# Kernel optimization log

Measured on AMD Instinct MI355X. Metric: run time of the kernel, lower is better.

The kernel has to match this reference:

```python
import jax, jax.numpy as jnp
import numpy as np

NB, H, C, HID, EMB = 4, 12, 1024, 768, 512
E, M, L, SPAN = 22, 4, 16, 32
TD, INTER = 20, 256
NN = E + E * M + L
NREL, NLAYERS = 3, 4

def _build_adj():
    # static relational adjacency: r0 entity<->its mentions, r1 mention<->co-entity mention, r2 mention<->link
    A = np.zeros((NREL, NN, NN), np.float32)
    for e in range(E):
        for m in range(M):
            mi = E + e * M + m
            A[0, e, mi] = A[0, mi, e] = 1.0
            for m2 in range(M):
                if m2 != m:
                    A[1, mi, E + e * M + m2] = 1.0
            li = E + E * M + ((e * M + m) % L)
            A[2, mi, li] = A[2, li, mi] = 1.0
    A = A / (A.sum(-1, keepdims=True) + 1e-5)
    return jnp.asarray(A)

_ADJ = _build_adj()
_TYPES = np.concatenate([np.zeros(E, np.int32), np.ones(E * M, np.int32), np.full(L, 2, np.int32)])

def _forward(sequence_output, attention, W_trans, b_trans, type_embed,
             rgcn_Wrel0, rgcn_Wself0, rgcn_Wrel, rgcn_Wself,
             fs_w1, fs_b1, fs_g1, fs_be1, fs_w2, fs_b2, fs_g2, fs_be2,
             fc_w1, fc_b1, fc_g1, fc_be1, fc_w2, fc_b2, fc_g2, fc_be2,
             cr_w1, cr_b1, cr_w2, cr_b2, cr_w3, cr_b3,
             mention_idx, link_start):
    n = sequence_output.shape[0]
    b = jnp.arange(n)[:, None, None]
    seq = sequence_output @ W_trans + b_trans            # [n,C,EMB] extractor_trans
    attq = attention.transpose(0, 2, 1, 3)               # [n,C,H,C] query-major
    # --- make_graph: mention / entity nodes (gather + logsumexp pooling) ---
    m_rep = seq[b, mention_idx]                          # [n,E,M,EMB]
    m_att = attq[b, mention_idx]                         # [n,E,M,H,C]
    e_rep = jax.nn.logsumexp(m_rep, axis=2)              # [n,E,EMB]
    e_att = m_att.mean(axis=2)                           # [n,E,H,C]
    # --- link nodes: attention-weighted span pooling ---
    idx = link_start[:, :, None] + jnp.arange(SPAN)      # [n,L,SPAN]
    span = seq[b, idx]                                   # [n,L,SPAN,EMB]
    att_rows = attq[b, idx]                              # [n,L,SPAN,H,C]
    col_idx = jnp.broadcast_to(idx[:, :, None, None, :], (n, L, SPAN, H, SPAN))
    block = jnp.take_along_axis(att_rows, col_idx, axis=4).mean(axis=3)  # [n,L,SPAN,SPAN]
    link_rep = jnp.einsum('nlst,nltd->nld', block, span) / SPAN          # [n,L,EMB]
    # --- node matrix + type embedding ---
    nodes = jnp.concatenate([e_rep, m_rep.reshape(n, E * M, EMB), link_rep], axis=1)
    tfeat = jnp.broadcast_to(type_embed[_TYPES][None], (n, NN, TD))
    h = jnp.concatenate([nodes, tfeat], axis=-1)         # [n,NN,EMB+TD]
    # --- RGCN ---
    def rgcn_layer(hh, Wrel, Wself):
        msg = jnp.einsum('rij,njd,rdo->nio', _ADJ, hh, Wrel)
        return jax.nn.relu(msg + hh @ Wself)
    h = rgcn_layer(h, rgcn_Wrel0, rgcn_Wself0)
    for l in range(NLAYERS - 1):
        h = rgcn_layer(h, rgcn_Wrel[l], rgcn_Wself[l])
    # --- relation_map: structure + attention-weighted context ---
    entity_stru = h[:, :E]                               # [n,E,EMB]
    ea = e_att.mean(axis=2)                              # [n,E,C]
    ea = ea / (ea.sum(-1, keepdims=True) + 1e-5)
    e_ctx = jnp.einsum('nec,ncd->ned', ea, seq)          # [n,E,EMB]
    ec = entity_stru + e_ctx
    fmap = (ec[:, :, None, :] * ec[:, None, :, :]).transpose(0, 3, 1, 2)  # [n,EMB,E,E]
    # --- SE fusion (fusion_s / fusion_c, BN in eval form) ---
    conv1x1 = lambda x, w, bb: jnp.einsum('nchw,oc->nohw', x, w) + bb[None, :, None, None]
    bn = lambda x, g, be: x * g[None, :, None, None] + be[None, :, None, None]
    s = bn(conv1x1(jax.nn.relu(bn(conv1x1(fmap, fs_w1, fs_b1), fs_g1, fs_be1)), fs_w2, fs_b2), fs_g2, fs_be2)
    pooled = fmap.mean(axis=(2, 3), keepdims=True)
    cb = bn(conv1x1(jax.nn.relu(bn(conv1x1(pooled, fc_w1, fc_b1), fc_g1, fc_be1)), fc_w2, fc_b2), fc_g2, fc_be2)
    fused = fmap * jax.nn.sigmoid(s + cb)
    # --- conv_reason 5x5 blocks ---
    dn = ('NCHW', 'OIHW', 'NCHW')
    conv = lambda x, w, bb: jax.lax.conv_general_dilated(x, w, (1, 1), 'SAME', dimension_numbers=dn) + bb[None, :, None, None]
    r = jax.nn.relu(conv(fused, cr_w1, cr_b1))
    r = jax.nn.relu(conv(r, cr_w2, cr_b2))
    return jax.nn.relu(conv(r, cr_w3, cr_b3))            # [n,EMB,E,E]

def setup_inputs():
    key = jax.random.key(0)
    ks = jax.random.split(key, 24)
    p = lambda k, sh: jax.random.normal(k, sh, jnp.float32) * 0.02
    z = lambda sh: jnp.zeros(sh, jnp.float32)
    o = lambda sh: jnp.ones(sh, jnp.float32)
    return {
        'sequence_output': jax.random.normal(ks[0], (NB, C, HID), jnp.float32),
        'attention': jax.random.uniform(ks[1], (NB, H, C, C), jnp.float32),
        'W_trans': p(ks[2], (HID, EMB)), 'b_trans': z((EMB,)),
        'type_embed': p(ks[3], (3, TD)),
        'rgcn_Wrel0': p(ks[4], (NREL, EMB + TD, EMB)), 'rgcn_Wself0': p(ks[5], (EMB + TD, EMB)),
        'rgcn_Wrel': p(ks[6], (NLAYERS - 1, NREL, EMB, EMB)), 'rgcn_Wself': p(ks[7], (NLAYERS - 1, EMB, EMB)),
        'fs_w1': p(ks[8], (INTER, EMB)), 'fs_b1': z((INTER,)), 'fs_g1': o((INTER,)), 'fs_be1': z((INTER,)),
        'fs_w2': p(ks[9], (EMB, INTER)), 'fs_b2': z((EMB,)), 'fs_g2': o((EMB,)), 'fs_be2': z((EMB,)),
        'fc_w1': p(ks[10], (INTER, EMB)), 'fc_b1': z((INTER,)), 'fc_g1': o((INTER,)), 'fc_be1': z((INTER,)),
        'fc_w2': p(ks[11], (EMB, INTER)), 'fc_b2': z((EMB,)), 'fc_g2': o((EMB,)), 'fc_be2': z((EMB,)),
        'cr_w1': p(ks[12], (INTER, EMB, 5, 5)), 'cr_b1': z((INTER,)),
        'cr_w2': p(ks[13], (INTER, INTER, 5, 5)), 'cr_b2': z((INTER,)),
        'cr_w3': p(ks[14], (EMB, INTER, 5, 5)), 'cr_b3': z((EMB,)),
        'mention_idx': jax.random.randint(ks[15], (NB, E, M), 0, C),
        'link_start': jnp.sort(jax.random.randint(ks[16], (NB, L), 0, C - SPAN), axis=-1),
    }

def reference(sequence_output, attention, W_trans, b_trans, type_embed,
              rgcn_Wrel0, rgcn_Wself0, rgcn_Wrel, rgcn_Wself,
              fs_w1, fs_b1, fs_g1, fs_be1, fs_w2, fs_b2, fs_g2, fs_be2,
              fc_w1, fc_b1, fc_g1, fc_be1, fc_w2, fc_b2, fc_g2, fc_be2,
              cr_w1, cr_b1, cr_w2, cr_b2, cr_w3, cr_b3,
              mention_idx, link_start):
    return _forward(sequence_output, attention, W_trans, b_trans, type_embed,
                    rgcn_Wrel0, rgcn_Wself0, rgcn_Wrel, rgcn_Wself,
                    fs_w1, fs_b1, fs_g1, fs_be1, fs_w2, fs_b2, fs_g2, fs_be2,
                    fc_w1, fc_b1, fc_g1, fc_be1, fc_w2, fc_b2, fc_g2, fc_be2,
                    cr_w1, cr_b1, cr_w2, cr_b2, cr_w3, cr_b3,
                    mention_idx, link_start)
```

## Files before the change

### kernel.cpp

```cpp
#include <hip/hip_runtime.h>
#include <hip/hip_bf16.h>
#include <stdint.h>

typedef long long ll;
typedef float f32x4 __attribute__((ext_vector_type(4)));
typedef __bf16 bf16x8 __attribute__((ext_vector_type(8)));
typedef __bf16 bf16x4 __attribute__((ext_vector_type(4)));


__global__ void k_cast_split(const float* __restrict__ in, __bf16* __restrict__ hi,
                             __bf16* __restrict__ lo, ll n){
  ll idx = (ll)blockIdx.x*256 + threadIdx.x;
  if (idx >= n) return;
  float x = in[idx];
  __bf16 h = (__bf16)x;
  hi[idx] = h; lo[idx] = (__bf16)(x - (float)h);
}
__global__ void k_cast_hi(const float* __restrict__ in, __bf16* __restrict__ hi, ll n){
  ll idx = (ll)blockIdx.x*256 + threadIdx.x;
  if (idx >= n) return;
  hi[idx] = (__bf16)in[idx];
}
__global__ void k_castT_split(const float* __restrict__ in, __bf16* __restrict__ hi,
                              __bf16* __restrict__ lo, int R, int C){
  ll idx = (ll)blockIdx.x*256 + threadIdx.x;
  if (idx >= (ll)R*C) return;
  int r = (int)(idx % R); int c = (int)(idx / R);
  float x = in[(ll)r*C + c];
  __bf16 h = (__bf16)x;
  hi[idx] = h; lo[idx] = (__bf16)(x - (float)h);
}

__global__ void k_wcatT2(const float* __restrict__ Wrel, const float* __restrict__ Wself,
                         __bf16* __restrict__ hi, __bf16* __restrict__ lo,
                         int Din, int Kpad){
  __shared__ float t[32][33];
  int l = blockIdx.z;
  const float* wr = Wrel + (ll)l*3*Din*512;
  const float* ws2 = Wself + (ll)l*Din*512;
  __bf16* hb = hi + (ll)l*512*Kpad;
  __bf16* lb = lo + (ll)l*512*Kpad;
  int k0 = blockIdx.x*32, o0 = blockIdx.y*32;
  int tx = threadIdx.x, ty = threadIdx.y;
  for (int j=ty; j<32; j+=8){
    int k = k0 + j; float v = 0.f;
    if (k < 3*Din) v = wr[(ll)k*512 + o0+tx];
    else if (k < 4*Din) v = ws2[(ll)(k-3*Din)*512 + o0+tx];
    t[j][tx] = v;
  }
  __syncthreads();
  for (int j=ty; j<32; j+=8){
    float x = t[tx][j];
    __bf16 h = (__bf16)x;
    hb[(ll)(o0+j)*Kpad + k0+tx] = h;
    lb[(ll)(o0+j)*Kpad + k0+tx] = (__bf16)(x - (float)h);
  }
}

__global__ void k_seqT(const float* __restrict__ seq, __bf16* __restrict__ hi,
                       __bf16* __restrict__ lo){
  __shared__ float t[32][33];
  int n = blockIdx.z;
  int r0 = blockIdx.x*32, c0 = blockIdx.y*32;
  int tx = threadIdx.x, ty = threadIdx.y;
  for (int j=ty; j<32; j+=8)
    t[j][tx] = seq[((ll)n*1024 + r0+j)*512 + c0+tx];
  __syncthreads();
  for (int j=ty; j<32; j+=8){
    float x = t[tx][j];
    __bf16 h = (__bf16)x;
    ll o = ((ll)n*512 + c0+j)*1024 + r0+tx;
    hi[o] = h; lo[o] = (__bf16)(x - (float)h);
  }
}

template<int SPLIT, int MODE, int BN>
__global__ __launch_bounds__(256) void gemm_mfma(
    const __bf16* __restrict__ Ahi, const __bf16* __restrict__ Alo,
    const __bf16* __restrict__ Bhi, const __bf16* __restrict__ Blo,
    float* __restrict__ Cf, __bf16* __restrict__ Cb,
    int M, int N, int K, ll sA, ll sB, ll sC,
    const float* __restrict__ biasN, const float* __restrict__ biasM,
    const float* __restrict__ gM, const float* __restrict__ beM)
{
  constexpr int BS = BN*64;
  constexpr int NF = BN/32;
  __shared__ bf16x8 lds8[((SPLIT?2:1)*(4096+BS))/16];
  char* lds = (char*)lds8;
  char* asH = lds;
  char* bsH = lds + 4096;
  char* asL = lds + 4096 + BS;
  char* bsL = lds + 8192 + BS;

  int b = blockIdx.z;
  Ahi += sA*b; Bhi += sB*b;
  if (SPLIT){ Alo += sA*b; Blo += sB*b; }

  const int tid = threadIdx.x;
  const int l15 = tid & 15, lg = (tid&63)>>4, lg16 = ((tid&63)>>4)*16;
  const int w = tid >> 6;
  const int wave_m0 = (w>>1)*32, wave_n0 = (w&1)*(BN/2);
  const int m0 = blockIdx.y*64, n0 = blockIdx.x*BN;

  const int sa_row = tid>>2, sa_c8 = tid&3;
  const int sa_byte = sa_row*64 + ((sa_c8*16) ^ (((sa_row>>1)&3)<<4));
  const int gmA = m0 + sa_row;

  int baseA[2], baseB[NF];
  #pragma unroll
  for (int mf=0; mf<2; ++mf){
    int r = wave_m0 + mf*16 + l15;
    baseA[mf] = r*64 + (lg16 ^ (((r>>1)&3)<<4));
  }
  #pragma unroll
  for (int nf=0; nf<NF; ++nf){
    int r = wave_n0 + nf*16 + l15;
    baseB[nf] = r*64 + (lg16 ^ (((r>>1)&3)<<4));
  }

  f32x4 acc[2][NF] = {};

  for (int k0=0; k0<K; k0+=32){
    __syncthreads();
    {
      bf16x8 v = {};
      if (gmA < M) v = *reinterpret_cast<const bf16x8*>(Ahi + (ll)gmA*K + k0 + sa_c8*8);
      *reinterpret_cast<bf16x8*>(asH + sa_byte) = v;
      if (SPLIT){
        bf16x8 vl = {};
        if (gmA < M) vl = *reinterpret_cast<const bf16x8*>(Alo + (ll)gmA*K + k0 + sa_c8*8);
        *reinterpret_cast<bf16x8*>(asL + sa_byte) = vl;
      }
    }
    #pragma unroll
    for (int i=0;i<BN/64;i++){
      int idx = tid + i*256;
      int row = idx>>2, c8 = idx&3;
      int gn = n0 + row;
      int byte = row*64 + ((c8*16) ^ (((row>>1)&3)<<4));
      bf16x8 v = {};
      if (gn < N) v = *reinterpret_cast<const bf16x8*>(Bhi + (ll)gn*K + k0 + c8*8);
      *reinterpret_cast<bf16x8*>(bsH + byte) = v;
      if (SPLIT){
        bf16x8 vl = {};
        if (gn < N) vl = *reinterpret_cast<const bf16x8*>(Blo + (ll)gn*K + k0 + c8*8);
        *reinterpret_cast<bf16x8*>(bsL + byte) = vl;
      }
    }
    __syncthreads();
    bf16x8 aH[2], bH[NF];
    #pragma unroll
    for (int mf=0; mf<2; ++mf) aH[mf] = *reinterpret_cast<const bf16x8*>(asH + baseA[mf]);
    #pragma unroll
    for (int nf=0; nf<NF; ++nf) bH[nf] = *reinterpret_cast<const bf16x8*>(bsH + baseB[nf]);
    if (SPLIT){
      bf16x8 aL[2], bL[NF];
      #pragma unroll
      for (int mf=0; mf<2; ++mf) aL[mf] = *reinterpret_cast<const bf16x8*>(asL + baseA[mf]);
      #pragma unroll
      for (int nf=0; nf<NF; ++nf) bL[nf] = *reinterpret_cast<const bf16x8*>(bsL + baseB[nf]);
      #pragma unroll
      for (int mf=0; mf<2; ++mf)
        #pragma unroll
        for (int nf=0; nf<NF; ++nf){
          acc[mf][nf] = __builtin_amdgcn_mfma_f32_16x16x32_bf16(aH[mf], bH[nf], acc[mf][nf], 0,0,0);
          acc[mf][nf] = __builtin_amdgcn_mfma_f32_16x16x32_bf16(aH[mf], bL[nf], acc[mf][nf], 0,0,0);
          acc[mf][nf] = __builtin_amdgcn_mfma_f32_16x16x32_bf16(aL[mf], bH[nf], acc[mf][nf], 0,0,0);
        }
    } else {
      #pragma unroll
      for (int mf=0; mf<2; ++mf)
        #pragma unroll
        for (int nf=0; nf<NF; ++nf)
          acc[mf][nf] = __builtin_amdgcn_mfma_f32_16x16x32_bf16(aH[mf], bH[nf], acc[mf][nf], 0,0,0);
    }
  }

  if (MODE==0 || MODE==1){
    float* C = Cf + sC*b;
    #pragma unroll
    for (int mf=0; mf<2; ++mf){
      int gmb = m0 + wave_m0 + mf*16 + lg*4;
      #pragma unroll
      for (int nf=0; nf<NF; ++nf){
        int gn = n0 + wave_n0 + nf*16 + l15;
        if (gn >= N) continue;
        float bn_ = (MODE==0 && biasN) ? biasN[gn] : 0.f;
        f32x4 a = acc[mf][nf];
        #pragma unroll
        for (int r=0;r<4;r++){
          int gm = gmb + r;
          if (gm < M){
            float v = a[r] + bn_;
            if (MODE==1) v = fmaxf(v, 0.f);
            C[(ll)gm*N + gn] = v;
          }
        }
      }
    }
  } else if (MODE==2){
    __bf16* C = Cb + sC*b;
    #pragma unroll
    for (int mf=0; mf<2; ++mf){
      int gmb = m0 + wave_m0 + mf*16 + lg*4;
      float b0=biasM[gmb], b1=biasM[gmb+1], b2=biasM[gmb+2], b3=biasM[gmb+3];
      float g0=gM[gmb], g1=gM[gmb+1], g2=gM[gmb+2], g3=gM[gmb+3];
      float e0=beM[gmb], e1=beM[gmb+1], e2=beM[gmb+2], e3=beM[gmb+3];
      #pragma unroll
      for (int nf=0; nf<NF; ++nf){
        int gn = n0 + wave_n0 + nf*16 + l15;
        if (gn >= N) continue;
        f32x4 a = acc[mf][nf];
        union { bf16x4 v; uint2 u; } pk;
        pk.v[0] = (__bf16)fmaxf((a[0]+b0)*g0+e0, 0.f);
        pk.v[1] = (__bf16)fmaxf((a[1]+b1)*g1+e1, 0.f);
        pk.v[2] = (__bf16)fmaxf((a[2]+b2)*g2+e2, 0.f);
        pk.v[3] = (__bf16)fmaxf((a[3]+b3)*g3+e3, 0.f);
        *reinterpret_cast<uint2*>(C + (ll)gn*M + gmb) = pk.u;
      }
    }
  } else {
    float* C = Cf + sC*b;
    #pragma unroll
    for (int mf=0; mf<2; ++mf){
      int gmb = m0 + wave_m0 + mf*16 + lg*4;
      float b0=biasM[gmb], b1=biasM[gmb+1], b2=biasM[gmb+2], b3=biasM[gmb+3];
      float g0=gM[gmb], g1=gM[gmb+1], g2=gM[gmb+2], g3=gM[gmb+3];
      float e0=beM[gmb], e1=beM[gmb+1], e2=beM[gmb+2], e3=beM[gmb+3];
      #pragma unroll
      for (int nf=0; nf<NF; ++nf){
        int gn = n0 + wave_n0 + nf*16 + l15;
        if (gn >= N) continue;
        f32x4 a = acc[mf][nf];
        C[(ll)(gmb+0)*N + gn] = (a[0]+b0)*g0+e0;
        C[(ll)(gmb+1)*N + gn] = (a[1]+b1)*g1+e1;
        C[(ll)(gmb+2)*N + gn] = (a[2]+b2)*g2+e2;
        C[(ll)(gmb+3)*N + gn] = (a[3]+b3)*g3+e3;
      }
    }
  }
}

template<int CIN, int OCHT, bool FINAL>
__global__ __launch_bounds__(256) void conv5_mfma(
    const __bf16* __restrict__ Xg, const __bf16* __restrict__ Wt,
    const float* __restrict__ bias, __bf16* __restrict__ Xout,
    float* __restrict__ outF)
{
  __shared__ bf16x8 Xs8[272*32/8];
  __shared__ bf16x8 Ws8[5*64*32/8];
  char* xs = (char*)Xs8;
  char* wsm = (char*)Ws8;

  const int tid = threadIdx.x;
  const int l = tid & 63;
  const int l15 = l & 15, lg = l >> 4, lg16 = (l>>4)*16;
  const int w = tid >> 6;
  const int wave_o0 = (w>>1)*32;
  const int wave_p0 = (w&1)*64;
  const int b = blockIdx.z;
  const int p0 = blockIdx.x*128;
  const int o0 = blockIdx.y*64;

  int orow0 = wave_o0 + l15;
  int orow1 = wave_o0 + 16 + l15;
  int baseA0 = orow0*64 + (lg16 ^ (((orow0>>1)&3)<<4));
  int baseA1 = orow1*64 + (lg16 ^ (((orow1>>1)&3)<<4));
  int pl[4];
  #pragma unroll
  for (int pf=0; pf<4; ++pf) pl[pf] = wave_p0 + pf*16 + l15;

  f32x4 acc[2][4] = {};

  const int NCB = CIN/32;
  for (int cblk=0; cblk<NCB; ++cblk){
    __syncthreads();
    #pragma unroll
    for (int i=0;i<5;i++){
      int idx = tid + i*256;
      if (idx < 1088){
        int e = idx>>2, c8 = idx&3;
        const __bf16* g = Xg + ((size_t)(b*928 + p0 + e))*CIN + cblk*32 + c8*8;
        bf16x8 v = *reinterpret_cast<const bf16x8*>(g);
        int byte = e*64 + ((c8*16) ^ (((e>>1)&3)<<4));
        *reinterpret_cast<bf16x8*>(xs + byte) = v;
      }
    }
    for (int g5=0; g5<5; ++g5){
      if (g5>0) __syncthreads();
      #pragma unroll
      for (int i=0;i<5;i++){
        int idx = tid + i*256;
        int tapL = idx>>8, r = idx&255;
        int o = r>>2, c8 = r&3;
        const __bf16* g = Wt + ((size_t)(o0+o)*25 + (g5*5+tapL))*CIN + cblk*32 + c8*8;
        bf16x8 v = *reinterpret_cast<const bf16x8*>(g);
        int byte = tapL*4096 + o*64 + ((c8*16) ^ (((o>>1)&3)<<4));
        *reinterpret_cast<bf16x8*>(wsm + byte) = v;
      }
      __syncthreads();
      #pragma unroll
      for (int tapL=0; tapL<5; ++tapL){
        bf16x8 a0 = *reinterpret_cast<const bf16x8*>(wsm + tapL*4096 + baseA0);
        bf16x8 a1 = *reinterpret_cast<const bf16x8*>(wsm + tapL*4096 + baseA1);
        int koff = g5*32 + tapL;
        #pragma unroll
        for (int pf=0; pf<4; ++pf){
          int e = pl[pf] + koff;
          bf16x8 bv = *reinterpret_cast<const bf16x8*>(xs + e*64 + (lg16 ^ (((e>>1)&3)<<4)));
          acc[0][pf] = __builtin_amdgcn_mfma_f32_16x16x32_bf16(a0, bv, acc[0][pf], 0,0,0);
          acc[1][pf] = __builtin_amdgcn_mfma_f32_16x16x32_bf16(a1, bv, acc[1][pf], 0,0,0);
        }
      }
    }
  }

  #pragma unroll
  for (int of=0; of<2; ++of){
    int og = o0 + wave_o0 + of*16 + lg*4;
    float b0 = bias[og], b1 = bias[og+1], b2 = bias[og+2], b3 = bias[og+3];
    #pragma unroll
    for (int pf=0; pf<4; ++pf){
      int p = p0 + pl[pf];
      int py = p>>5, px = p&31;
      if (py>=22 || px>=22) continue;
      f32x4 a = acc[of][pf];
      float v0 = fmaxf(a[0]+b0, 0.f), v1 = fmaxf(a[1]+b1, 0.f);
      float v2 = fmaxf(a[2]+b2, 0.f), v3 = fmaxf(a[3]+b3, 0.f);
      if (FINAL){
        size_t base = ((size_t)b*OCHT + og)*484 + py*22 + px;
        outF[base] = v0; outF[base+484] = v1; outF[base+968] = v2; outF[base+1452] = v3;
      } else {
        union { bf16x4 v; uint2 u; } pk;
        pk.v[0] = (__bf16)v0; pk.v[1] = (__bf16)v1; pk.v[2] = (__bf16)v2; pk.v[3] = (__bf16)v3;
        int e = p + 66;
        *reinterpret_cast<uint2*>(Xout + ((size_t)(b*928 + e))*OCHT + og) = pk.u;
      }
    }
  }
}

__global__ void wt_make(const float* __restrict__ w, __bf16* __restrict__ wt, int C){
  int o = blockIdx.x;
  for (int c=threadIdx.x; c<C; c+=256){
    const float* src = w + ((size_t)o*C + c)*25;
    float v[25];
    #pragma unroll
    for (int t=0;t<25;t++) v[t] = src[t];
    #pragma unroll
    for (int t=0;t<25;t++) wt[((size_t)o*25 + t)*C + c] = (__bf16)v[t];
  }
}

__global__ void k_ent(const float* __restrict__ seq, const int* __restrict__ midx, float* __restrict__ h0){
  int n = blockIdx.x/22, e = blockIdx.x%22;
  int rows[4];
  #pragma unroll
  for (int m=0;m<4;m++) rows[m] = midx[(n*22+e)*4+m];
  for (int d=threadIdx.x; d<512; d+=256){
    float v[4]; float mx = -1e30f;
    #pragma unroll
    for (int m=0;m<4;m++){
      v[m] = seq[((ll)n*1024+rows[m])*512 + d];
      h0[((ll)n*126+22+e*4+m)*532 + d] = v[m];
      mx = fmaxf(mx, v[m]);
    }
    float s = 0.f;
    #pragma unroll
    for (int m=0;m<4;m++) s += expf(v[m]-mx);
    h0[((ll)n*126+e)*532 + d] = mx + logf(s);
  }
}

__global__ void k_link(const float* __restrict__ att, const float* __restrict__ seq,
                       const int* __restrict__ ls_, float* __restrict__ h0){
  int n = blockIdx.x/16, l = blockIdx.x%16;
  int ls = ls_[n*16+l];
  int t = threadIdx.x; int tt = t>>3, lane = t&7;
  __shared__ float part[32][8];
  __shared__ float wv[32];
  float acc = 0.f;
  for (int i=lane; i<384; i+=8){
    int h = i>>5, s = i&31;
    acc += att[((ll)(n*12+h)*1024 + ls+s)*1024 + (ls+tt)];
  }
  part[tt][lane] = acc; __syncthreads();
  if (lane==0){
    float s2=0.f;
    #pragma unroll
    for (int q=0;q<8;q++) s2 += part[tt][q];
    wv[tt] = s2*(1.f/12.f);
  }
  __syncthreads();
  for (int d=t; d<512; d+=256){
    float a2 = 0.f;
    for (int tk=0;tk<32;tk++) a2 += wv[tk]*seq[((ll)n*1024+ls+tk)*512 + d];
    h0[((ll)n*126+110+l)*532 + d] = a2*(1.f/32.f);
  }
}

__global__ void k_tfeat(const float* __restrict__ te, float* __restrict__ h0){
  int idx = blockIdx.x*256 + threadIdx.x;
  if (idx >= 4*126*20) return;
  int t = idx%20; int i = (idx/20)%126; int n = idx/(20*126);
  int ty = (i<22)?0:((i<110)?1:2);
  h0[((ll)n*126+i)*532 + 512 + t] = te[ty*20+t];
}

__global__ void k_ea1(const float* __restrict__ att, const int* __restrict__ midx,
                      float* __restrict__ eap){
  int b = blockIdx.x;
  int h = b%12; int e = (b/12)%22; int n = b/(12*22);
  int rows[4];
  #pragma unroll
  for (int m=0;m<4;m++) rows[m] = midx[(n*22+e)*4+m];
  const float* base = att + (ll)(n*12+h)*1024*1024;
  for (int c=threadIdx.x; c<1024; c+=256){
    float acc = 0.f;
    #pragma unroll
    for (int m=0;m<4;m++) acc += base[(ll)rows[m]*1024 + c];
    eap[(ll)b*1024 + c] = acc;
  }
}
__global__ void k_ea2(const float* __restrict__ eap, float* __restrict__ ea){
  int b = blockIdx.x; int t = threadIdx.x;
  __shared__ float vals[1024];
  __shared__ float red[256];
  float local = 0.f;
  for (int c=t; c<1024; c+=256){
    float s = 0.f;
    #pragma unroll
    for (int h=0;h<12;h++) s += eap[(ll)(b*12+h)*1024 + c];
    s *= (1.f/48.f);
    vals[c] = s; local += s;
  }
  red[t] = local; __syncthreads();
  for (int s=128;s>0;s>>=1){ if (t<s) red[t]+=red[t+s]; __syncthreads(); }
  float denom = red[0] + 1e-5f;
  for (int c=t; c<1024; c+=256) ea[(ll)b*1024 + c] = vals[c]/denom;
}

__global__ void k_buildX_s(const float* __restrict__ h,
                           __bf16* __restrict__ Xhi, __bf16* __restrict__ Xlo,
                           int Din, int ldX){
  int n = blockIdx.x/126, i = blockIdx.x%126;
  const float* hb = h + (ll)n*126*Din;
  ll rowoff = (ll)(n*126+i)*ldX;
  const float inv1 = 1.f/(1.f+1e-5f), inv3 = 1.f/(3.f+1e-5f), inv4 = 1.f/(4.f+1e-5f);
  for (int d=threadIdx.x; d<Din; d+=256){
    float m0v=0.f, m1v=0.f, m2v=0.f;
    if (i < 22){
      int base = 22 + i*4;
      float s = hb[(ll)(base+0)*Din+d] + hb[(ll)(base+1)*Din+d]
              + hb[(ll)(base+2)*Din+d] + hb[(ll)(base+3)*Din+d];
      m0v = s * inv4;
    } else if (i < 110){
      int em = i-22, e = em>>2, base = 22+(e<<2);
      m0v = hb[(ll)e*Din+d] * inv1;
      float s1 = 0.f;
      #pragma unroll
      for (int m2=0;m2<4;m2++) if (base+m2 != i) s1 += hb[(ll)(base+m2)*Din+d];
      m1v = s1 * inv3;
      m2v = hb[(ll)(110+(em&15))*Din+d] * inv1;
    } else {
      int li0 = i-110;
      int cnt = (li0<8)?6:5;
      float s = 0.f;
      for (int t2=0;t2<cnt;t2++) s += hb[(ll)(22+li0+16*t2)*Din+d];
      m2v = s / ((float)cnt + 1e-5f);
    }
    float hh = hb[(ll)i*Din+d];
    float v4[4] = {m0v, m1v, m2v, hh};
    #pragma unroll
    for (int r=0;r<4;r++){
      __bf16 hi = (__bf16)v4[r];
      Xhi[rowoff + r*Din + d] = hi;
      Xlo[rowoff + r*Din + d] = (__bf16)(v4[r] - (float)hi);
    }
  }
  for (int k=4*Din+threadIdx.x; k<ldX; k+=256){
    Xhi[rowoff + k] = (__bf16)0.f;
    Xlo[rowoff + k] = (__bf16)0.f;
  }
}

__global__ void k_ec(const float* __restrict__ hfin, const float* __restrict__ ectx, float* __restrict__ ec){
  int idx = blockIdx.x*256 + threadIdx.x;
  int d = idx & 511; int e = (idx>>9)%22; int n = idx/(22*512);
  ec[idx] = hfin[((ll)n*126+e)*512 + d] + ectx[idx];
}

__global__ void k_fmapT(const float* __restrict__ ec, __bf16* __restrict__ fmapT){
  int idx = blockIdx.x*256 + threadIdx.x;
  int ch = idx & 511; int p = (idx>>9) % 484; int n = idx/(484*512);
  int i = p/22, j = p%22;
  float v = ec[((ll)n*22+i)*512+ch] * ec[((ll)n*22+j)*512+ch];
  fmapT[idx] = (__bf16)v;
}

__global__ void k_pool(const float* __restrict__ ec, float* __restrict__ pooled){
  int idx = blockIdx.x*256 + threadIdx.x;
  if (idx >= 2048) return;
  int n = idx>>9, c = idx&511;
  float s = 0.f;
  for (int i=0;i<22;i++) s += ec[((ll)n*22+i)*512 + c];
  pooled[idx] = s*s*(1.f/484.f);
}

__global__ void k_cb(const float* __restrict__ pooled,
                     const float* __restrict__ w1, const float* __restrict__ b1,
                     const float* __restrict__ g1, const float* __restrict__ be1,
                     const float* __restrict__ w2, const float* __restrict__ b2,
                     const float* __restrict__ g2, const float* __restrict__ be2,
                     float* __restrict__ cb){
  int n = blockIdx.x; int t = threadIdx.x;
  __shared__ float ps[512], t1[256];
  for (int c=t; c<512; c+=256) ps[c] = pooled[n*512+c];
  __syncthreads();
  {
    float acc = 0.f;
    for (int c=0;c<512;c++) acc += w1[t*512+c]*ps[c];
    float v = g1[t]*(acc+b1[t]) + be1[t];
    t1[t] = fmaxf(v, 0.f);
  }
  __syncthreads();
  for (int o=t; o<512; o+=256){
    float acc = 0.f;
    for (int c=0;c<256;c++) acc += w2[o*256+c]*t1[c];
    cb[n*512+o] = g2[o]*(acc+b2[o]) + be2[o];
  }
}

__global__ void k_fused_b(const __bf16* __restrict__ fmapT, const float* __restrict__ sb,
                          const float* __restrict__ cbv, __bf16* __restrict__ Xint1){
  int n = blockIdx.z; int d8 = blockIdx.y;
  int p = blockIdx.x*256 + threadIdx.x;
  if (p >= 484) return;
  int py = p/22, px = p%22;
  int e = (py+2)*32 + px + 2;
  bf16x8 fm = *reinterpret_cast<const bf16x8*>(fmapT + ((ll)(n*484+p))*512 + d8*8);
  union { bf16x8 v; uint4 u; } pk;
  #pragma unroll
  for (int di=0; di<8; ++di){
    float sv = sb[((ll)n*512 + d8*8 + di)*484 + p] + cbv[n*512 + d8*8 + di];
    float sg = 1.f/(1.f + expf(-sv));
    pk.v[di] = (__bf16)((float)fm[di]*sg);
  }
  *reinterpret_cast<uint4*>(Xint1 + ((size_t)(n*928 + e))*512 + d8*8) = pk.u;
}

extern "C" void kernel_launch(void* const* d_in, const int* in_sizes, int n_in,
                              void* d_out, int out_size, void* d_ws, size_t ws_size,
                              hipStream_t stream)
{
  (void)in_sizes; (void)n_in; (void)out_size; (void)ws_size;
  const float* seqout   = (const float*)d_in[0];
  const float* att      = (const float*)d_in[1];
  const float* W_trans  = (const float*)d_in[2];
  const float* b_trans  = (const float*)d_in[3];
  const float* type_emb = (const float*)d_in[4];
  const float* Wrel0    = (const float*)d_in[5];
  const float* Wself0   = (const float*)d_in[6];
  const float* Wrel     = (const float*)d_in[7];
  const float* Wself    = (const float*)d_in[8];
  const float* fs_w1    = (const float*)d_in[9];
  const float* fs_b1    = (const float*)d_in[10];
  const float* fs_g1    = (const float*)d_in[11];
  const float* fs_be1   = (const float*)d_in[12];
  const float* fs_w2    = (const float*)d_in[13];
  const float* fs_b2    = (const float*)d_in[14];
  const float* fs_g2    = (const float*)d_in[15];
  const float* fs_be2   = (const float*)d_in[16];
  const float* fc_w1    = (const float*)d_in[17];
  const float* fc_b1    = (const float*)d_in[18];
  const float* fc_g1    = (const float*)d_in[19];
  const float* fc_be1   = (const float*)d_in[20];
  const float* fc_w2    = (const float*)d_in[21];
  const float* fc_b2    = (const float*)d_in[22];
  const float* fc_g2    = (const float*)d_in[23];
  const float* fc_be2   = (const float*)d_in[24];
  const float* cr_w1    = (const float*)d_in[25];
  const float* cr_b1    = (const float*)d_in[26];
  const float* cr_w2    = (const float*)d_in[27];
  const float* cr_b2    = (const float*)d_in[28];
  const float* cr_w3    = (const float*)d_in[29];
  const float* cr_b3    = (const float*)d_in[30];
  const int*   midx     = (const int*)d_in[31];
  const int*   lstart   = (const int*)d_in[32];
  float* out            = (float*)d_out;

  char* wsb = (char*)d_ws;
  size_t off = 0;
  auto allocB = [&](size_t nbytes)->char*{ char* p = wsb + off; off += (nbytes + 63) & ~(size_t)63; return p; };
  float* seq   = (float*)allocB((size_t)4096*512*4);
  float* h0    = (float*)allocB((size_t)504*532*4);
  float* eap   = (float*)allocB((size_t)4224*1024*4);
  float* ea    = (float*)allocB((size_t)88*1024*4);
  float* ectx  = (float*)allocB((size_t)88*512*4);
  float* hA    = (float*)allocB((size_t)504*512*4);
  float* hB    = (float*)allocB((size_t)504*512*4);
  float* ec    = (float*)allocB((size_t)88*512*4);
  float* sb    = (float*)allocB((size_t)4*512*484*4);
  float* pooled= (float*)allocB(2048*4);
  float* cbv   = (float*)allocB(2048*4);
  __bf16* sqh  = (__bf16*)allocB((size_t)4096*768*2);
  __bf16* sql  = (__bf16*)allocB((size_t)4096*768*2);
  __bf16* wth  = (__bf16*)allocB((size_t)512*768*2);
  __bf16* wtl  = (__bf16*)allocB((size_t)512*768*2);
  __bf16* sqTh = (__bf16*)allocB((size_t)4*512*1024*2);
  __bf16* sqTl = (__bf16*)allocB((size_t)4*512*1024*2);
  __bf16* eah  = (__bf16*)allocB((size_t)88*1024*2);
  __bf16* eal  = (__bf16*)allocB((size_t)88*1024*2);
  __bf16* Xhi  = (__bf16*)allocB((size_t)504*2144*2);
  __bf16* Xlo  = (__bf16*)allocB((size_t)504*2144*2);
  __bf16* wc0h = (__bf16*)allocB((size_t)512*2144*2);
  __bf16* wc0l = (__bf16*)allocB((size_t)512*2144*2);
  __bf16* wc13h= (__bf16*)allocB((size_t)3*512*2048*2);
  __bf16* wc13l= (__bf16*)allocB((size_t)3*512*2048*2);
  __bf16* fmapT= (__bf16*)allocB((size_t)4*484*512*2);
  __bf16* s1bT = (__bf16*)allocB((size_t)4*484*256*2);
  __bf16* w1b  = (__bf16*)allocB((size_t)256*512*2);
  __bf16* w2b  = (__bf16*)allocB((size_t)512*256*2);
  __bf16* Xint1 = (__bf16*)allocB((size_t)4*928*512*2);
  __bf16* Xint2 = (__bf16*)allocB((size_t)4*928*256*2);
  __bf16* Xint3 = (__bf16*)allocB((size_t)4*928*256*2);
  __bf16* Wt1   = (__bf16*)allocB((size_t)256*25*512*2);
  __bf16* Wt2   = (__bf16*)allocB((size_t)256*25*256*2);
  __bf16* Wt3   = (__bf16*)allocB((size_t)512*25*256*2);

  (void)hipMemsetAsync(Xint1, 0, (size_t)4*928*512*2, stream);
  (void)hipMemsetAsync(Xint2, 0, (size_t)4*928*256*2, stream);
  (void)hipMemsetAsync(Xint3, 0, (size_t)4*928*256*2, stream);

  wt_make<<<256,256,0,stream>>>(cr_w1, Wt1, 512);
  wt_make<<<256,256,0,stream>>>(cr_w2, Wt2, 256);
  wt_make<<<512,256,0,stream>>>(cr_w3, Wt3, 256);
  k_cast_split<<<12288,256,0,stream>>>(seqout, sqh, sql, (ll)4096*768);
  k_castT_split<<<1536,256,0,stream>>>(W_trans, wth, wtl, 768, 512);
  k_cast_hi<<<512,256,0,stream>>>(fs_w1, w1b, 256*512);
  k_cast_hi<<<512,256,0,stream>>>(fs_w2, w2b, 512*256);
  k_wcatT2<<<dim3(67,16,1),dim3(32,8),0,stream>>>(Wrel0, Wself0, wc0h, wc0l, 532, 2144);
  k_wcatT2<<<dim3(64,16,3),dim3(32,8),0,stream>>>(Wrel, Wself, wc13h, wc13l, 512, 2048);

  gemm_mfma<1,0,128><<<dim3(4,64,1),256,0,stream>>>(sqh, sql, wth, wtl, seq, nullptr,
                                                    4096,512,768, 0,0,0, b_trans,nullptr,nullptr,nullptr);
  k_ent <<<88,256,0,stream>>>(seq, midx, h0);
  k_link<<<64,256,0,stream>>>(att, seq, lstart, h0);
  k_tfeat<<<40,256,0,stream>>>(type_emb, h0);
  k_ea1<<<1056,256,0,stream>>>(att, midx, eap);
  k_ea2<<<88,256,0,stream>>>(eap, ea);
  k_seqT<<<dim3(32,16,4),dim3(32,8),0,stream>>>(seq, sqTh, sqTl);
  k_cast_split<<<352,256,0,stream>>>(ea, eah, eal, (ll)88*1024);
  gemm_mfma<1,0,64><<<dim3(8,1,4),256,0,stream>>>(eah, eal, sqTh, sqTl, ectx, nullptr,
                                                  22,512,1024, (ll)22*1024, (ll)512*1024, (ll)22*512,
                                                  nullptr,nullptr,nullptr,nullptr);
  k_buildX_s<<<504,256,0,stream>>>(h0, Xhi, Xlo, 532, 2144);
  gemm_mfma<1,1,64><<<dim3(8,8,1),256,0,stream>>>(Xhi, Xlo, wc0h, wc0l, hA, nullptr,
                                                  504,512,2144, 0,0,0, nullptr,nullptr,nullptr,nullptr);
  float* hcur = hA; float* hnxt = hB;
  for (int l=0;l<3;l++){
    k_buildX_s<<<504,256,0,stream>>>(hcur, Xhi, Xlo, 512, 2048);
    gemm_mfma<1,1,64><<<dim3(8,8,1),256,0,stream>>>(Xhi, Xlo,
                                                    wc13h + (ll)l*512*2048, wc13l + (ll)l*512*2048,
                                                    hnxt, nullptr,
                                                    504,512,2048, 0,0,0, nullptr,nullptr,nullptr,nullptr);
    float* t = hcur; hcur = hnxt; hnxt = t;
  }
  k_ec<<<176,256,0,stream>>>(hcur, ectx, ec);
  k_fmapT<<<3872,256,0,stream>>>(ec, fmapT);
  gemm_mfma<0,2,64><<<dim3(8,4,4),256,0,stream>>>(w1b, nullptr, fmapT, nullptr, nullptr, s1bT,
                                                  256,484,512, 0, (ll)484*512, (ll)484*256,
                                                  nullptr, fs_b1, fs_g1, fs_be1);
  gemm_mfma<0,3,64><<<dim3(8,8,4),256,0,stream>>>(w2b, nullptr, s1bT, nullptr, sb, nullptr,
                                                  512,484,256, 0, (ll)484*256, (ll)512*484,
                                                  nullptr, fs_b2, fs_g2, fs_be2);
  k_pool<<<8,256,0,stream>>>(ec, pooled);
  k_cb<<<4,256,0,stream>>>(pooled, fc_w1, fc_b1, fc_g1, fc_be1,
                           fc_w2, fc_b2, fc_g2, fc_be2, cbv);
  k_fused_b<<<dim3(2,64,4),256,0,stream>>>(fmapT, sb, cbv, Xint1);
  conv5_mfma<512,256,false><<<dim3(6,4,4),256,0,stream>>>(Xint1, Wt1, cr_b1, Xint2, nullptr);
  conv5_mfma<256,256,false><<<dim3(6,4,4),256,0,stream>>>(Xint2, Wt2, cr_b2, Xint3, nullptr);
  conv5_mfma<256,512,true ><<<dim3(6,8,4),256,0,stream>>>(Xint3, Wt3, cr_b3, nullptr, out);
}
```

Measured before the change: 653.0 us.

## Fuse fp32-to-bf16 split casts into GEMM, add intra-block split-K, merge small kernels

The GEMM now reads fp32 A directly and splits it into hi/lo bf16 in registers, which removes the separate cast kernels and their intermediate buffers. It runs 512 threads as two K-slices and reduces the partial sums through LDS. Several small kernels are merged: the three weight transposes, the node builders, the two entity-attention passes, and pool with the channel branch. The sigmoid gate and padded scatter are fused into the second spatial GEMM epilogue. The trade-offs are extra A conversion work repeated across N tiles and an LDS reduction step, in exchange for fewer launches and less memory traffic.

```diff
diff --git a/kernel.cpp b/kernel.cpp
--- a/kernel.cpp
+++ b/kernel.cpp
@@ -7,20 +7,6 @@
 typedef __bf16 bf16x8 __attribute__((ext_vector_type(8)));
 typedef __bf16 bf16x4 __attribute__((ext_vector_type(4)));
 
-
-__global__ void k_cast_split(const float* __restrict__ in, __bf16* __restrict__ hi,
-                             __bf16* __restrict__ lo, ll n){
-  ll idx = (ll)blockIdx.x*256 + threadIdx.x;
-  if (idx >= n) return;
-  float x = in[idx];
-  __bf16 h = (__bf16)x;
-  hi[idx] = h; lo[idx] = (__bf16)(x - (float)h);
-}
-__global__ void k_cast_hi(const float* __restrict__ in, __bf16* __restrict__ hi, ll n){
-  ll idx = (ll)blockIdx.x*256 + threadIdx.x;
-  if (idx >= n) return;
-  hi[idx] = (__bf16)in[idx];
-}
 __global__ void k_castT_split(const float* __restrict__ in, __bf16* __restrict__ hi,
                               __bf16* __restrict__ lo, int R, int C){
   ll idx = (ll)blockIdx.x*256 + threadIdx.x;
@@ -74,35 +60,58 @@
   }
 }
 
+__global__ void wt_make_all(const float* __restrict__ w1, const float* __restrict__ w2,
+                            const float* __restrict__ w3, __bf16* __restrict__ d1,
+                            __bf16* __restrict__ d2, __bf16* __restrict__ d3){
+  int b = blockIdx.x;
+  const float* w; __bf16* dst; int C, o;
+  if (b < 256){ w=w1; dst=d1; C=512; o=b; }
+  else if (b < 512){ w=w2; dst=d2; C=256; o=b-256; }
+  else { w=w3; dst=d3; C=256; o=b-512; }
+  for (int c=threadIdx.x; c<C; c+=256){
+    const float* src = w + ((size_t)o*C + c)*25;
+    float v[25];
+    #pragma unroll
+    for (int t=0;t<25;t++) v[t] = src[t];
+    #pragma unroll
+    for (int t=0;t<25;t++) dst[((size_t)o*25 + t)*C + c] = (__bf16)v[t];
+  }
+}
+
 template<int SPLIT, int MODE, int BN>
-__global__ __launch_bounds__(256) void gemm_mfma(
-    const __bf16* __restrict__ Ahi, const __bf16* __restrict__ Alo,
+__global__ __launch_bounds__(512) void gemm_mfma(
+    const float* __restrict__ A,
     const __bf16* __restrict__ Bhi, const __bf16* __restrict__ Blo,
     float* __restrict__ Cf, __bf16* __restrict__ Cb,
     int M, int N, int K, ll sA, ll sB, ll sC,
     const float* __restrict__ biasN, const float* __restrict__ biasM,
-    const float* __restrict__ gM, const float* __restrict__ beM)
+    const float* __restrict__ gM, const float* __restrict__ beM,
+    const __bf16* __restrict__ Fm, const float* __restrict__ CBV)
 {
-  constexpr int BS = BN*64;
   constexpr int NF = BN/32;
-  __shared__ bf16x8 lds8[((SPLIT?2:1)*(4096+BS))/16];
-  char* lds = (char*)lds8;
-  char* asH = lds;
-  char* bsH = lds + 4096;
-  char* asL = lds + 4096 + BS;
-  char* bsL = lds + 8192 + BS;
+  constexpr int SL = (4096 + BN*64) * (SPLIT?2:1);
+  constexpr int REDB = 256*2*NF*16;
+  constexpr int LDSB = (2*SL > REDB) ? 2*SL : REDB;
+  __shared__ char lds[LDSB];
 
   int b = blockIdx.z;
-  Ahi += sA*b; Bhi += sB*b;
-  if (SPLIT){ Alo += sA*b; Blo += sB*b; }
+  A += sA*b; Bhi += sB*b; if (SPLIT) Blo += sB*b;
 
   const int tid = threadIdx.x;
-  const int l15 = tid & 15, lg = (tid&63)>>4, lg16 = ((tid&63)>>4)*16;
-  const int w = tid >> 6;
-  const int wave_m0 = (w>>1)*32, wave_n0 = (w&1)*(BN/2);
+  const int slice = tid>>8;
+  const int tl = tid & 255;
+  const int w4 = (tid>>6)&3;
+  const int grp = tid>>8;
+  const int l15 = tid&15, lg=(tid&63)>>4, lg16=lg*16;
+  const int wave_m0=(w4>>1)*32, wave_n0=(w4&1)*(BN/2);
   const int m0 = blockIdx.y*64, n0 = blockIdx.x*BN;
 
-  const int sa_row = tid>>2, sa_c8 = tid&3;
+  char* sA_H = lds + slice*SL;
+  char* sB_H = sA_H + 4096;
+  char* sA_L = sB_H + BN*64;
+  char* sB_L = sA_L + 4096;
+
+  const int sa_row=tl>>2, sa_c8=tl&3;
   const int sa_byte = sa_row*64 + ((sa_c8*16) ^ (((sa_row>>1)&3)<<4));
   const int gmA = m0 + sa_row;
 
@@ -120,45 +129,53 @@
 
   f32x4 acc[2][NF] = {};
 
-  for (int k0=0; k0<K; k0+=32){
+  for (int k0=0; k0<K; k0+=64){
+    int kk = k0 + slice*32;
     __syncthreads();
     {
-      bf16x8 v = {};
-      if (gmA < M) v = *reinterpret_cast<const bf16x8*>(Ahi + (ll)gmA*K + k0 + sa_c8*8);
-      *reinterpret_cast<bf16x8*>(asH + sa_byte) = v;
-      if (SPLIT){
-        bf16x8 vl = {};
-        if (gmA < M) vl = *reinterpret_cast<const bf16x8*>(Alo + (ll)gmA*K + k0 + sa_c8*8);
-        *reinterpret_cast<bf16x8*>(asL + sa_byte) = vl;
-      }
+      float f[8] = {0,0,0,0,0,0,0,0};
+      if (gmA < M){
+        float4 p0 = *reinterpret_cast<const float4*>(A + (ll)gmA*K + kk + sa_c8*8);
+        float4 p1 = *reinterpret_cast<const float4*>(A + (ll)gmA*K + kk + sa_c8*8 + 4);
+        f[0]=p0.x; f[1]=p0.y; f[2]=p0.z; f[3]=p0.w;
+        f[4]=p1.x; f[5]=p1.y; f[6]=p1.z; f[7]=p1.w;
+      }
+      bf16x8 h, l;
+      #pragma unroll
+      for (int j=0;j<8;j++){
+        h[j] = (__bf16)f[j];
+        if (SPLIT) l[j] = (__bf16)(f[j] - (float)h[j]);
+      }
+      *reinterpret_cast<bf16x8*>(sA_H + sa_byte) = h;
+      if (SPLIT) *reinterpret_cast<bf16x8*>(sA_L + sa_byte) = l;
     }
     #pragma unroll
     for (int i=0;i<BN/64;i++){
-      int idx = tid + i*256;
+      int idx = tl + i*256;
       int row = idx>>2, c8 = idx&3;
       int gn = n0 + row;
       int byte = row*64 + ((c8*16) ^ (((row>>1)&3)<<4));
       bf16x8 v = {};
-      if (gn < N) v = *reinterpret_cast<const bf16x8*>(Bhi + (ll)gn*K + k0 + c8*8);
-      *reinterpret_cast<bf16x8*>(bsH + byte) = v;
+      if (gn < N) v = *reinterpret_cast<const bf16x8*>(Bhi + (ll)gn*K + kk + c8*8);
+      *reinterpret_cast<bf16x8*>(sB_H + byte) = v;
       if (SPLIT){
         bf16x8 vl = {};
-        if (gn < N) vl = *reinterpret_cast<const bf16x8*>(Blo + (ll)gn*K + k0 + c8*8);
-        *reinterpret_cast<bf16x8*>(bsL + byte) = vl;
+        if (gn < N) vl = *reinterpret_cast<const bf16x8*>(Blo + (ll)gn*K + kk + c8*8);
+        *reinterpret_cast<bf16x8*>(sB_L + byte) = vl;
       }
     }
     __syncthreads();
     bf16x8 aH[2], bH[NF];
     #pragma unroll
-    for (int mf=0; mf<2; ++mf) aH[mf] = *reinterpret_cast<const bf16x8*>(asH + baseA[mf]);
-    #pragma unroll
-    for (int nf=0; nf<NF; ++nf) bH[nf] = *reinterpret_cast<const bf16x8*>(bsH + baseB[nf]);
+    for (int mf=0; mf<2; ++mf) aH[mf] = *reinterpret_cast<const bf16x8*>(sA_H + baseA[mf]);
+    #pragma unroll
+    for (int nf=0; nf<NF; ++nf) bH[nf] = *reinterpret_cast<const bf16x8*>(sB_H + baseB[nf]);
     if (SPLIT){
       bf16x8 aL[2], bL[NF];
       #pragma unroll
-      for (int mf=0; mf<2; ++mf) aL[mf] = *reinterpret_cast<const bf16x8*>(asL + baseA[mf]);
-      #pragma unroll
-      for (int nf=0; nf<NF; ++nf) bL[nf] = *reinterpret_cast<const bf16x8*>(bsL + baseB[nf]);
+      for (int mf=0; mf<2; ++mf) aL[mf] = *reinterpret_cast<const bf16x8*>(sA_L + baseA[mf]);
+      #pragma unroll
+      for (int nf=0; nf<NF; ++nf) bL[nf] = *reinterpret_cast<const bf16x8*>(sB_L + baseB[nf]);
       #pragma unroll
       for (int mf=0; mf<2; ++mf)
         #pragma unroll
@@ -174,6 +191,26 @@
         for (int nf=0; nf<NF; ++nf)
           acc[mf][nf] = __builtin_amdgcn_mfma_f32_16x16x32_bf16(aH[mf], bH[nf], acc[mf][nf], 0,0,0);
     }
+  }
+
+  __syncthreads();
+  if (grp==1){
+    char* rp = lds + (ll)(tid-256)*(2*NF*16);
+    #pragma unroll
+    for (int mf=0; mf<2; ++mf)
+      #pragma unroll
+      for (int nf=0; nf<NF; ++nf)
+        *reinterpret_cast<f32x4*>(rp + (mf*NF+nf)*16) = acc[mf][nf];
+  }
+  __syncthreads();
+  if (grp!=0) return;
+  {
+    char* rp = lds + (ll)tid*(2*NF*16);
+    #pragma unroll
+    for (int mf=0; mf<2; ++mf)
+      #pragma unroll
+      for (int nf=0; nf<NF; ++nf)
+        acc[mf][nf] += *reinterpret_cast<f32x4*>(rp + (mf*NF+nf)*16);
   }
 
   if (MODE==0 || MODE==1){
@@ -220,22 +257,34 @@
       }
     }
   } else {
-    float* C = Cf + sC*b;
+    __bf16* C = Cb + sC*b;
+    const __bf16* fm = Fm + (ll)b*484*512;
+    const float* cb = CBV + (ll)b*512;
     #pragma unroll
     for (int mf=0; mf<2; ++mf){
       int gmb = m0 + wave_m0 + mf*16 + lg*4;
       float b0=biasM[gmb], b1=biasM[gmb+1], b2=biasM[gmb+2], b3=biasM[gmb+3];
       float g0=gM[gmb], g1=gM[gmb+1], g2=gM[gmb+2], g3=gM[gmb+3];
       float e0=beM[gmb], e1=beM[gmb+1], e2=beM[gmb+2], e3=beM[gmb+3];
+      float c0=cb[gmb], c1=cb[gmb+1], c2=cb[gmb+2], c3=cb[gmb+3];
       #pragma unroll
       for (int nf=0; nf<NF; ++nf){
         int gn = n0 + wave_n0 + nf*16 + l15;
         if (gn >= N) continue;
         f32x4 a = acc[mf][nf];
-        C[(ll)(gmb+0)*N + gn] = (a[0]+b0)*g0+e0;
-        C[(ll)(gmb+1)*N + gn] = (a[1]+b1)*g1+e1;
-        C[(ll)(gmb+2)*N + gn] = (a[2]+b2)*g2+e2;
-        C[(ll)(gmb+3)*N + gn] = (a[3]+b3)*g3+e3;
+        bf16x4 fmv = *reinterpret_cast<const bf16x4*>(fm + (ll)gn*512 + gmb);
+        float s0 = (a[0]+b0)*g0+e0 + c0;
+        float s1 = (a[1]+b1)*g1+e1 + c1;
+        float s2 = (a[2]+b2)*g2+e2 + c2;
+        float s3 = (a[3]+b3)*g3+e3 + c3;
+        union { bf16x4 v; uint2 u; } pk;
+        pk.v[0] = (__bf16)((float)fmv[0] / (1.f + expf(-s0)));
+        pk.v[1] = (__bf16)((float)fmv[1] / (1.f + expf(-s1)));
+        pk.v[2] = (__bf16)((float)fmv[2] / (1.f + expf(-s2)));
+        pk.v[3] = (__bf16)((float)fmv[3] / (1.f + expf(-s3)));
+        int py = gn/22, px = gn%22;
+        int e = (py+2)*32 + px + 2;
+        *reinterpret_cast<uint2*>(C + (ll)e*512 + gmb) = pk.u;
       }
     }
   }
@@ -340,108 +389,89 @@
   }
 }
 
-__global__ void wt_make(const float* __restrict__ w, __bf16* __restrict__ wt, int C){
-  int o = blockIdx.x;
-  for (int c=threadIdx.x; c<C; c+=256){
-    const float* src = w + ((size_t)o*C + c)*25;
-    float v[25];
-    #pragma unroll
-    for (int t=0;t<25;t++) v[t] = src[t];
-    #pragma unroll
-    for (int t=0;t<25;t++) wt[((size_t)o*25 + t)*C + c] = (__bf16)v[t];
-  }
-}
-
-__global__ void k_ent(const float* __restrict__ seq, const int* __restrict__ midx, float* __restrict__ h0){
+__global__ void k_nodes(const float* __restrict__ seq, const float* __restrict__ att,
+                        const int* __restrict__ midx, const int* __restrict__ ls_,
+                        const float* __restrict__ te, float* __restrict__ h0){
+  __shared__ float part[32][8];
+  __shared__ float wv[32];
+  int b = blockIdx.x;
+  if (b < 88){
+    int n = b/22, e = b%22;
+    int rows[4];
+    #pragma unroll
+    for (int m=0;m<4;m++) rows[m] = midx[(n*22+e)*4+m];
+    for (int d=threadIdx.x; d<512; d+=256){
+      float v[4]; float mx = -1e30f;
+      #pragma unroll
+      for (int m=0;m<4;m++){
+        v[m] = seq[((ll)n*1024+rows[m])*512 + d];
+        h0[((ll)n*126+22+e*4+m)*532 + d] = v[m];
+        mx = fmaxf(mx, v[m]);
+      }
+      float s = 0.f;
+      #pragma unroll
+      for (int m=0;m<4;m++) s += expf(v[m]-mx);
+      h0[((ll)n*126+e)*532 + d] = mx + logf(s);
+    }
+  } else if (b < 152){
+    int bb = b-88;
+    int n = bb/16, l = bb%16;
+    int ls = ls_[n*16+l];
+    int t = threadIdx.x; int tt = t>>3, lane = t&7;
+    float acc = 0.f;
+    for (int i=lane; i<384; i+=8){
+      int h = i>>5, s = i&31;
+      acc += att[((ll)(n*12+h)*1024 + ls+s)*1024 + (ls+tt)];
+    }
+    part[tt][lane] = acc; __syncthreads();
+    if (lane==0){
+      float s2=0.f;
+      #pragma unroll
+      for (int q=0;q<8;q++) s2 += part[tt][q];
+      wv[tt] = s2*(1.f/12.f);
+    }
+    __syncthreads();
+    for (int d=t; d<512; d+=256){
+      float a2 = 0.f;
+      for (int tk=0;tk<32;tk++) a2 += wv[tk]*seq[((ll)n*1024+ls+tk)*512 + d];
+      h0[((ll)n*126+110+l)*532 + d] = a2*(1.f/32.f);
+    }
+  } else {
+    int idx = (b-152)*256 + threadIdx.x;
+    if (idx < 4*126*20){
+      int t = idx%20; int i = (idx/20)%126; int n = idx/(20*126);
+      int ty = (i<22)?0:((i<110)?1:2);
+      h0[((ll)n*126+i)*532 + 512 + t] = te[ty*20+t];
+    }
+  }
+}
+
+__global__ void k_ea(const float* __restrict__ att, const int* __restrict__ midx, float* __restrict__ ea){
   int n = blockIdx.x/22, e = blockIdx.x%22;
+  int t = threadIdx.x;
+  __shared__ float vals[1024];
+  __shared__ float red[256];
   int rows[4];
   #pragma unroll
   for (int m=0;m<4;m++) rows[m] = midx[(n*22+e)*4+m];
-  for (int d=threadIdx.x; d<512; d+=256){
-    float v[4]; float mx = -1e30f;
-    #pragma unroll
-    for (int m=0;m<4;m++){
-      v[m] = seq[((ll)n*1024+rows[m])*512 + d];
-      h0[((ll)n*126+22+e*4+m)*532 + d] = v[m];
-      mx = fmaxf(mx, v[m]);
-    }
-    float s = 0.f;
-    #pragma unroll
-    for (int m=0;m<4;m++) s += expf(v[m]-mx);
-    h0[((ll)n*126+e)*532 + d] = mx + logf(s);
-  }
-}
-
-__global__ void k_link(const float* __restrict__ att, const float* __restrict__ seq,
-                       const int* __restrict__ ls_, float* __restrict__ h0){
-  int n = blockIdx.x/16, l = blockIdx.x%16;
-  int ls = ls_[n*16+l];
-  int t = threadIdx.x; int tt = t>>3, lane = t&7;
-  __shared__ float part[32][8];
-  __shared__ float wv[32];
-  float acc = 0.f;
-  for (int i=lane; i<384; i+=8){
-    int h = i>>5, s = i&31;
-    acc += att[((ll)(n*12+h)*1024 + ls+s)*1024 + (ls+tt)];
-  }
-  part[tt][lane] = acc; __syncthreads();
-  if (lane==0){
-    float s2=0.f;
-    #pragma unroll
-    for (int q=0;q<8;q++) s2 += part[tt][q];
-    wv[tt] = s2*(1.f/12.f);
-  }
-  __syncthreads();
-  for (int d=t; d<512; d+=256){
-    float a2 = 0.f;
-    for (int tk=0;tk<32;tk++) a2 += wv[tk]*seq[((ll)n*1024+ls+tk)*512 + d];
-    h0[((ll)n*126+110+l)*532 + d] = a2*(1.f/32.f);
-  }
-}
-
-__global__ void k_tfeat(const float* __restrict__ te, float* __restrict__ h0){
-  int idx = blockIdx.x*256 + threadIdx.x;
-  if (idx >= 4*126*20) return;
-  int t = idx%20; int i = (idx/20)%126; int n = idx/(20*126);
-  int ty = (i<22)?0:((i<110)?1:2);
-  h0[((ll)n*126+i)*532 + 512 + t] = te[ty*20+t];
-}
-
-__global__ void k_ea1(const float* __restrict__ att, const int* __restrict__ midx,
-                      float* __restrict__ eap){
-  int b = blockIdx.x;
-  int h = b%12; int e = (b/12)%22; int n = b/(12*22);
-  int rows[4];
-  #pragma unroll
-  for (int m=0;m<4;m++) rows[m] = midx[(n*22+e)*4+m];
-  const float* base = att + (ll)(n*12+h)*1024*1024;
-  for (int c=threadIdx.x; c<1024; c+=256){
-    float acc = 0.f;
-    #pragma unroll
-    for (int m=0;m<4;m++) acc += base[(ll)rows[m]*1024 + c];
-    eap[(ll)b*1024 + c] = acc;
-  }
-}
-__global__ void k_ea2(const float* __restrict__ eap, float* __restrict__ ea){
-  int b = blockIdx.x; int t = threadIdx.x;
-  __shared__ float vals[1024];
-  __shared__ float red[256];
   float local = 0.f;
   for (int c=t; c<1024; c+=256){
-    float s = 0.f;
-    #pragma unroll
-    for (int h=0;h<12;h++) s += eap[(ll)(b*12+h)*1024 + c];
-    s *= (1.f/48.f);
-    vals[c] = s; local += s;
+    float acc = 0.f;
+    #pragma unroll
+    for (int m=0;m<4;m++){
+      const float* base = att + ((ll)n*12*1024 + rows[m])*1024 + c;
+      for (int h=0;h<12;h++) acc += base[(ll)h*1024*1024];
+    }
+    acc *= (1.f/48.f);
+    vals[c] = acc; local += acc;
   }
   red[t] = local; __syncthreads();
   for (int s=128;s>0;s>>=1){ if (t<s) red[t]+=red[t+s]; __syncthreads(); }
   float denom = red[0] + 1e-5f;
-  for (int c=t; c<1024; c+=256) ea[(ll)b*1024 + c] = vals[c]/denom;
-}
-
-__global__ void k_buildX_s(const float* __restrict__ h,
-                           __bf16* __restrict__ Xhi, __bf16* __restrict__ Xlo,
+  for (int c=t; c<1024; c+=256) ea[((ll)n*22+e)*1024 + c] = vals[c]/denom;
+}
+
+__global__ void k_buildX_s(const float* __restrict__ h, float* __restrict__ X,
                            int Din, int ldX){
   int n = blockIdx.x/126, i = blockIdx.x%126;
   const float* hb = h + (ll)n*126*Din;
@@ -470,18 +500,12 @@
       m2v = s / ((float)cnt + 1e-5f);
     }
     float hh = hb[(ll)i*Din+d];
-    float v4[4] = {m0v, m1v, m2v, hh};
-    #pragma unroll
-    for (int r=0;r<4;r++){
-      __bf16 hi = (__bf16)v4[r];
-      Xhi[rowoff + r*Din + d] = hi;
-      Xlo[rowoff + r*Din + d] = (__bf16)(v4[r] - (float)hi);
-    }
-  }
-  for (int k=4*Din+threadIdx.x; k<ldX; k+=256){
-    Xhi[rowoff + k] = (__bf16)0.f;
-    Xlo[rowoff + k] = (__bf16)0.f;
-  }
+    X[rowoff + 0*Din + d] = m0v;
+    X[rowoff + 1*Din + d] = m1v;
+    X[rowoff + 2*Din + d] = m2v;
+    X[rowoff + 3*Din + d] = hh;
+  }
+  for (int k=4*Din+threadIdx.x; k<ldX; k+=256) X[rowoff + k] = 0.f;
 }
 
 __global__ void k_ec(const float* __restrict__ hfin, const float* __restrict__ ectx, float* __restrict__ ec){
@@ -498,24 +522,19 @@
   fmapT[idx] = (__bf16)v;
 }
 
-__global__ void k_pool(const float* __restrict__ ec, float* __restrict__ pooled){
-  int idx = blockIdx.x*256 + threadIdx.x;
-  if (idx >= 2048) return;
-  int n = idx>>9, c = idx&511;
-  float s = 0.f;
-  for (int i=0;i<22;i++) s += ec[((ll)n*22+i)*512 + c];
-  pooled[idx] = s*s*(1.f/484.f);
-}
-
-__global__ void k_cb(const float* __restrict__ pooled,
-                     const float* __restrict__ w1, const float* __restrict__ b1,
-                     const float* __restrict__ g1, const float* __restrict__ be1,
-                     const float* __restrict__ w2, const float* __restrict__ b2,
-                     const float* __restrict__ g2, const float* __restrict__ be2,
-                     float* __restrict__ cb){
+__global__ void k_poolcb(const float* __restrict__ ec,
+                         const float* __restrict__ w1, const float* __restrict__ b1,
+                         const float* __restrict__ g1, const float* __restrict__ be1,
+                         const float* __restrict__ w2, const float* __restrict__ b2,
+                         const float* __restrict__ g2, const float* __restrict__ be2,
+                         float* __restrict__ cb){
   int n = blockIdx.x; int t = threadIdx.x;
   __shared__ float ps[512], t1[256];
-  for (int c=t; c<512; c+=256) ps[c] = pooled[n*512+c];
+  for (int c=t; c<512; c+=256){
+    float s = 0.f;
+    for (int i=0;i<22;i++) s += ec[((ll)n*22+i)*512 + c];
+    ps[c] = s*s*(1.f/484.f);
+  }
   __syncthreads();
   {
     float acc = 0.f;
@@ -529,24 +548,6 @@
     for (int c=0;c<256;c++) acc += w2[o*256+c]*t1[c];
     cb[n*512+o] = g2[o]*(acc+b2[o]) + be2[o];
   }
-}
-
-__global__ void k_fused_b(const __bf16* __restrict__ fmapT, const float* __restrict__ sb,
-                          const float* __restrict__ cbv, __bf16* __restrict__ Xint1){
-  int n = blockIdx.z; int d8 = blockIdx.y;
-  int p = blockIdx.x*256 + threadIdx.x;
-  if (p >= 484) return;
-  int py = p/22, px = p%22;
-  int e = (py+2)*32 + px + 2;
-  bf16x8 fm = *reinterpret_cast<const bf16x8*>(fmapT + ((ll)(n*484+p))*512 + d8*8);
-  union { bf16x8 v; uint4 u; } pk;
-  #pragma unroll
-  for (int di=0; di<8; ++di){
-    float sv = sb[((ll)n*512 + d8*8 + di)*484 + p] + cbv[n*512 + d8*8 + di];
-    float sg = 1.f/(1.f + expf(-sv));
-    pk.v[di] = (__bf16)((float)fm[di]*sg);
-  }
-  *reinterpret_cast<uint4*>(Xint1 + ((size_t)(n*928 + e))*512 + d8*8) = pk.u;
 }
 
 extern "C" void kernel_launch(void* const* d_in, const int* in_sizes, int n_in,
@@ -594,33 +595,23 @@
   auto allocB = [&](size_t nbytes)->char*{ char* p = wsb + off; off += (nbytes + 63) & ~(size_t)63; return p; };
   float* seq   = (float*)allocB((size_t)4096*512*4);
   float* h0    = (float*)allocB((size_t)504*532*4);
-  float* eap   = (float*)allocB((size_t)4224*1024*4);
   float* ea    = (float*)allocB((size_t)88*1024*4);
   float* ectx  = (float*)allocB((size_t)88*512*4);
+  float* X     = (float*)allocB((size_t)504*2176*4);
   float* hA    = (float*)allocB((size_t)504*512*4);
   float* hB    = (float*)allocB((size_t)504*512*4);
   float* ec    = (float*)allocB((size_t)88*512*4);
-  float* sb    = (float*)allocB((size_t)4*512*484*4);
-  float* pooled= (float*)allocB(2048*4);
   float* cbv   = (float*)allocB(2048*4);
-  __bf16* sqh  = (__bf16*)allocB((size_t)4096*768*2);
-  __bf16* sql  = (__bf16*)allocB((size_t)4096*768*2);
   __bf16* wth  = (__bf16*)allocB((size_t)512*768*2);
   __bf16* wtl  = (__bf16*)allocB((size_t)512*768*2);
   __bf16* sqTh = (__bf16*)allocB((size_t)4*512*1024*2);
   __bf16* sqTl = (__bf16*)allocB((size_t)4*512*1024*2);
-  __bf16* eah  = (__bf16*)allocB((size_t)88*1024*2);
-  __bf16* eal  = (__bf16*)allocB((size_t)88*1024*2);
-  __bf16* Xhi  = (__bf16*)allocB((size_t)504*2144*2);
-  __bf16* Xlo  = (__bf16*)allocB((size_t)504*2144*2);
-  __bf16* wc0h = (__bf16*)allocB((size_t)512*2144*2);
-  __bf16* wc0l = (__bf16*)allocB((size_t)512*2144*2);
+  __bf16* wc0h = (__bf16*)allocB((size_t)512*2176*2);
+  __bf16* wc0l = (__bf16*)allocB((size_t)512*2176*2);
   __bf16* wc13h= (__bf16*)allocB((size_t)3*512*2048*2);
   __bf16* wc13l= (__bf16*)allocB((size_t)3*512*2048*2);
   __bf16* fmapT= (__bf16*)allocB((size_t)4*484*512*2);
   __bf16* s1bT = (__bf16*)allocB((size_t)4*484*256*2);
-  __bf16* w1b  = (__bf16*)allocB((size_t)256*512*2);
-  __bf16* w2b  = (__bf16*)allocB((size_t)512*256*2);
   __bf16* Xint1 = (__bf16*)allocB((size_t)4*928*512*2);
   __bf16* Xint2 = (__bf16*)allocB((size_t)4*928*256*2);
   __bf16* Xint3 = (__bf16*)allocB((size_t)4*928*256*2);
@@ -628,56 +619,42 @@
   __bf16* Wt2   = (__bf16*)allocB((size_t)256*25*256*2);
   __bf16* Wt3   = (__bf16*)allocB((size_t)512*25*256*2);
 
-  (void)hipMemsetAsync(Xint1, 0, (size_t)4*928*512*2, stream);
-  (void)hipMemsetAsync(Xint2, 0, (size_t)4*928*256*2, stream);
-  (void)hipMemsetAsync(Xint3, 0, (size_t)4*928*256*2, stream);
-
-  wt_make<<<256,256,0,stream>>>(cr_w1, Wt1, 512);
-  wt_make<<<256,256,0,stream>>>(cr_w2, Wt2, 256);
-  wt_make<<<512,256,0,stream>>>(cr_w3, Wt3, 256);
-  k_cast_split<<<12288,256,0,stream>>>(seqout, sqh, sql, (ll)4096*768);
+  (void)hipMemsetAsync(Xint1, 0, (size_t)(4*928*512 + 4*928*256 + 4*928*256)*2, stream);
+
+  wt_make_all<<<1024,256,0,stream>>>(cr_w1, cr_w2, cr_w3, Wt1, Wt2, Wt3);
   k_castT_split<<<1536,256,0,stream>>>(W_trans, wth, wtl, 768, 512);
-  k_cast_hi<<<512,256,0,stream>>>(fs_w1, w1b, 256*512);
-  k_cast_hi<<<512,256,0,stream>>>(fs_w2, w2b, 512*256);
-  k_wcatT2<<<dim3(67,16,1),dim3(32,8),0,stream>>>(Wrel0, Wself0, wc0h, wc0l, 532, 2144);
+  k_wcatT2<<<dim3(68,16,1),dim3(32,8),0,stream>>>(Wrel0, Wself0, wc0h, wc0l, 532, 2176);
   k_wcatT2<<<dim3(64,16,3),dim3(32,8),0,stream>>>(Wrel, Wself, wc13h, wc13l, 512, 2048);
 
-  gemm_mfma<1,0,128><<<dim3(4,64,1),256,0,stream>>>(sqh, sql, wth, wtl, seq, nullptr,
-                                                    4096,512,768, 0,0,0, b_trans,nullptr,nullptr,nullptr);
-  k_ent <<<88,256,0,stream>>>(seq, midx, h0);
-  k_link<<<64,256,0,stream>>>(att, seq, lstart, h0);
-  k_tfeat<<<40,256,0,stream>>>(type_emb, h0);
-  k_ea1<<<1056,256,0,stream>>>(att, midx, eap);
-  k_ea2<<<88,256,0,stream>>>(eap, ea);
+  gemm_mfma<1,0,128><<<dim3(4,64,1),512,0,stream>>>(seqout, wth, wtl, seq, nullptr,
+      4096,512,768, 0,0,0, b_trans,nullptr,nullptr,nullptr, nullptr,nullptr);
+  k_nodes<<<192,256,0,stream>>>(seq, att, midx, lstart, type_emb, h0);
+  k_ea<<<88,256,0,stream>>>(att, midx, ea);
   k_seqT<<<dim3(32,16,4),dim3(32,8),0,stream>>>(seq, sqTh, sqTl);
-  k_cast_split<<<352,256,0,stream>>>(ea, eah, eal, (ll)88*1024);
-  gemm_mfma<1,0,64><<<dim3(8,1,4),256,0,stream>>>(eah, eal, sqTh, sqTl, ectx, nullptr,
-                                                  22,512,1024, (ll)22*1024, (ll)512*1024, (ll)22*512,
-                                                  nullptr,nullptr,nullptr,nullptr);
-  k_buildX_s<<<504,256,0,stream>>>(h0, Xhi, Xlo, 532, 2144);
-  gemm_mfma<1,1,64><<<dim3(8,8,1),256,0,stream>>>(Xhi, Xlo, wc0h, wc0l, hA, nullptr,
-                                                  504,512,2144, 0,0,0, nullptr,nullptr,nullptr,nullptr);
+  gemm_mfma<1,0,64><<<dim3(8,1,4),512,0,stream>>>(ea, sqTh, sqTl, ectx, nullptr,
+      22,512,1024, (ll)22*1024, (ll)512*1024, (ll)22*512,
+      nullptr,nullptr,nullptr,nullptr, nullptr,nullptr);
+  k_buildX_s<<<504,256,0,stream>>>(h0, X, 532, 2176);
+  gemm_mfma<1,1,64><<<dim3(8,8,1),512,0,stream>>>(X, wc0h, wc0l, hA, nullptr,
+      504,512,2176, 0,0,0, nullptr,nullptr,nullptr,nullptr, nullptr,nullptr);
   float* hcur = hA; float* hnxt = hB;
   for (int l=0;l<3;l++){
-    k_buildX_s<<<504,256,0,stream>>>(hcur, Xhi, Xlo, 512, 2048);
-    gemm_mfma<1,1,64><<<dim3(8,8,1),256,0,stream>>>(Xhi, Xlo,
-                                                    wc13h + (ll)l*512*2048, wc13l + (ll)l*512*2048,
-                                                    hnxt, nullptr,
-                                                    504,512,2048, 0,0,0, nullptr,nullptr,nullptr,nullptr);
+    k_buildX_s<<<504,256,0,stream>>>(hcur, X, 512, 2048);
+    gemm_mfma<1,1,64><<<dim3(8,8,1),512,0,stream>>>(X,
+        wc13h + (ll)l*512*2048, wc13l + (ll)l*512*2048, hnxt, nullptr,
+        504,512,2048, 0,0,0, nullptr,nullptr,nullptr,nullptr, nullptr,nullptr);
     float* t = hcur; hcur = hnxt; hnxt = t;
   }
   k_ec<<<176,256,0,stream>>>(hcur, ectx, ec);
   k_fmapT<<<3872,256,0,stream>>>(ec, fmapT);
-  gemm_mfma<0,2,64><<<dim3(8,4,4),256,0,stream>>>(w1b, nullptr, fmapT, nullptr, nullptr, s1bT,
-                                                  256,484,512, 0, (ll)484*512, (ll)484*256,
-                                                  nullptr, fs_b1, fs_g1, fs_be1);
-  gemm_mfma<0,3,64><<<dim3(8,8,4),256,0,stream>>>(w2b, nullptr, s1bT, nullptr, sb, nullptr,
-                                                  512,484,256, 0, (ll)484*256, (ll)512*484,
-                                                  nullptr, fs_b2, fs_g2, fs_be2);
-  k_pool<<<8,256,0,stream>>>(ec, pooled);
-  k_cb<<<4,256,0,stream>>>(pooled, fc_w1, fc_b1, fc_g1, fc_be1,
-                           fc_w2, fc_b2, fc_g2, fc_be2, cbv);
-  k_fused_b<<<dim3(2,64,4),256,0,stream>>>(fmapT, sb, cbv, Xint1);
+  gemm_mfma<0,2,64><<<dim3(8,4,4),512,0,stream>>>(fs_w1, fmapT, nullptr, nullptr, s1bT,
+      256,484,512, 0, (ll)484*512, (ll)484*256,
+      nullptr, fs_b1, fs_g1, fs_be1, nullptr,nullptr);
+  k_poolcb<<<4,256,0,stream>>>(ec, fc_w1, fc_b1, fc_g1, fc_be1,
+                               fc_w2, fc_b2, fc_g2, fc_be2, cbv);
+  gemm_mfma<0,4,64><<<dim3(8,8,4),512,0,stream>>>(fs_w2, s1bT, nullptr, nullptr, Xint1,
+      512,484,256, 0, (ll)484*256, (ll)928*512,
+      nullptr, fs_b2, fs_g2, fs_be2, fmapT, cbv);
   conv5_mfma<512,256,false><<<dim3(6,4,4),256,0,stream>>>(Xint1, Wt1, cr_b1, Xint2, nullptr);
   conv5_mfma<256,256,false><<<dim3(6,4,4),256,0,stream>>>(Xint2, Wt2, cr_b2, Xint3, nullptr);
   conv5_mfma<256,512,true ><<<dim3(6,8,4),256,0,stream>>>(Xint3, Wt3, cr_b3, nullptr, out);
```

Result: faster. 554.2 us (-15.1%).
